# Kernel tuning notes

Hardware: AMD Instinct MI355X
Metric: run time of the kernel (lower is better)

Reference implementation:

```python
import jax, jax.numpy as jnp
import numpy as np

N_NODES = 100000
N_EDGES = 1200000
IN_CH = 64
HID = 64


def sage_conv(x, src, dst, Wl, b, Wr, num_nodes):
    # mean aggregation of source-node features at target nodes (flow=source_to_target)
    msg = x[src]                                      # [E, C] gather
    agg = jax.ops.segment_sum(msg, dst, num_segments=num_nodes)  # [N, C]
    cnt = jax.ops.segment_sum(jnp.ones((src.shape[0],), x.dtype), dst,
                              num_segments=num_nodes)
    mean = agg / jnp.maximum(cnt, 1.0)[:, None]
    # PyG SAGEConv: lin_l(aggregated) + bias + lin_r(root)
    return mean @ Wl + b + x @ Wr


def setup_inputs() -> dict:
    key = jax.random.key(0)
    ks = jax.random.split(key, 10)
    x = jax.random.normal(ks[0], (N_NODES, IN_CH), dtype=jnp.float32)
    edge_index = jax.random.randint(ks[1], (2, N_EDGES), 0, N_NODES, dtype=jnp.int64)
    s1 = 1.0 / np.sqrt(IN_CH)
    s2 = 1.0 / np.sqrt(HID)
    W1l = jax.random.uniform(ks[2], (IN_CH, HID), jnp.float32, -s1, s1)
    b1 = jax.random.uniform(ks[3], (HID,), jnp.float32, -s1, s1)
    W1r = jax.random.uniform(ks[4], (IN_CH, HID), jnp.float32, -s1, s1)
    W2l = jax.random.uniform(ks[5], (HID, HID), jnp.float32, -s2, s2)
    b2 = jax.random.uniform(ks[6], (HID,), jnp.float32, -s2, s2)
    W2r = jax.random.uniform(ks[7], (HID, HID), jnp.float32, -s2, s2)
    Wfc = jax.random.uniform(ks[8], (HID, 1), jnp.float32, -s2, s2)
    bfc = jax.random.uniform(ks[9], (1,), jnp.float32, -s2, s2)
    return {"x": x, "edge_index": edge_index, "W1l": W1l, "b1": b1, "W1r": W1r,
            "W2l": W2l, "b2": b2, "W2r": W2r, "Wfc": Wfc, "bfc": bfc}


def reference(x, edge_index, W1l, b1, W1r, W2l, b2, W2r, Wfc, bfc):
    num_nodes = x.shape[0]
    src, dst = edge_index[0], edge_index[1]
    x = jnp.nan_to_num(x, nan=0.0)
    # layer 1: SAGEConv -> ReLU (dropout is identity in eval)
    h = jax.nn.relu(sage_conv(x, src, dst, W1l, b1, W1r, num_nodes))
    # layer 2
    h = jax.nn.relu(sage_conv(h, src, dst, W2l, b2, W2r, num_nodes))
    pred = (h @ Wfc + bfc)[:, 0]  # (num_nodes,)
    return pred
```

## Files before the change

### kernel.cpp

```cpp
#include <hip/hip_runtime.h>

#define NN_NODES 100000
#define NN_EDGES 1200000
#define CH 64
#define BUCKET_NODES 200
#define NBUCKETS (NN_NODES / BUCKET_NODES)
#define EPB 4096
#define PREP_THREADS 1024
#define XCDS 8
#define PCAP 768
#define BMAX (XCDS * PCAP)

#define PA_BLOCKS ((NN_EDGES + EPB - 1) / EPB)
#define CV_ITEMS (NN_NODES * CH / 4)
#define CV_BLOCKS ((CV_ITEMS + PREP_THREADS - 1) / PREP_THREADS)
#define WP_ITEMS (64 * 128)
#define WP_BLOCKS ((WP_ITEMS + PREP_THREADS - 1) / PREP_THREADS)

typedef __attribute__((ext_vector_type(8))) short bf16x8;
typedef __attribute__((ext_vector_type(4))) float f32x4;

__device__ __forceinline__ float nan0(float v) { return v == v ? v : 0.0f; }

__device__ __forceinline__ unsigned short f2bf(float f) {
    unsigned u = __float_as_uint(f);
    return (unsigned short)((u + 0x7fffu + ((u >> 16) & 1u)) >> 16);
}

__device__ __forceinline__ unsigned xcc_id() {
    unsigned x;
    asm volatile("s_getreg_b32 %0, hwreg(HW_REG_XCC_ID)" : "=s"(x));
    return x & (XCDS - 1);
}

__global__ __launch_bounds__(PREP_THREADS) void prep_kernel(
    const float* __restrict__ x, unsigned short* __restrict__ xb,
    const float* __restrict__ W1l, const float* __restrict__ W1r,
    const float* __restrict__ W2l, const float* __restrict__ W2r,
    unsigned short* __restrict__ Wt1, unsigned short* __restrict__ Wt2,
    const int* __restrict__ src, const int* __restrict__ dst,
    int* __restrict__ bcnt, unsigned int* __restrict__ bbuf)
{
    __shared__ int lhist[NBUCKETS];
    __shared__ int lbase[NBUCKETS];
    int tid = threadIdx.x;
    int bid = blockIdx.x;

    if (bid < PA_BLOCKS) {
        int e0 = bid * EPB;
        unsigned xcc = xcc_id();

        for (int i = tid; i < NBUCKETS; i += PREP_THREADS) lhist[i] = 0;
        __syncthreads();

        int eb = e0 + tid * 4;
        int nv = NN_EDGES - eb;
        if (nv > 4) nv = 4;
        int da[4] = {-1, -1, -1, -1};
        if (nv == 4) {
            int4 dv = *(const int4*)(dst + eb);
            da[0] = dv.x; da[1] = dv.y; da[2] = dv.z; da[3] = dv.w;
        } else {
            for (int r = 0; r < nv; r++) da[r] = dst[eb + r];
        }
        #pragma unroll
        for (int r = 0; r < 4; r++)
            if (da[r] >= 0) atomicAdd(&lhist[da[r] / BUCKET_NODES], 1);
        __syncthreads();

        for (int i = tid; i < NBUCKETS; i += PREP_THREADS) {
            int c = lhist[i];
            lbase[i] = c > 0 ? atomicAdd(&bcnt[i * XCDS + xcc], c) : 0;
            lhist[i] = 0;
        }
        __syncthreads();

        int sa[4] = {0, 0, 0, 0};
        if (nv == 4) {
            int4 sv = *(const int4*)(src + eb);
            sa[0] = sv.x; sa[1] = sv.y; sa[2] = sv.z; sa[3] = sv.w;
        } else {
            for (int r = 0; r < nv; r++) sa[r] = src[eb + r];
        }
        #pragma unroll
        for (int r = 0; r < 4; r++) {
            int d = da[r];
            if (d >= 0) {
                int b = d / BUCKET_NODES;
                int dloc = d - b * BUCKET_NODES;
                int pos = lbase[b] + atomicAdd(&lhist[b], 1);
                if (pos < PCAP)
                    bbuf[((size_t)b * XCDS + xcc) * PCAP + pos] =
                        ((unsigned)dloc << 24) | (unsigned)sa[r];
            }
        }
    } else if (bid < PA_BLOCKS + CV_BLOCKS) {
        int i = (bid - PA_BLOCKS) * PREP_THREADS + tid;
        if (i < CV_ITEMS) {
            float4 v = ((const float4*)x)[i];
            v.x = nan0(v.x); v.y = nan0(v.y); v.z = nan0(v.z); v.w = nan0(v.w);
            ushort4 o;
            o.x = f2bf(v.x); o.y = f2bf(v.y); o.z = f2bf(v.z); o.w = f2bf(v.w);
            ((ushort4*)xb)[i] = o;
        }
    } else {
        int i = (bid - PA_BLOCKS - CV_BLOCKS) * PREP_THREADS + tid;
        if (i < WP_ITEMS) {
            int n = i >> 7;
            int k = i & 127;
            float v1 = (k < 64) ? W1l[k * 64 + n] : W1r[(k - 64) * 64 + n];
            float v2 = (k < 64) ? W2l[k * 64 + n] : W2r[(k - 64) * 64 + n];
            Wt1[i] = f2bf(v1);
            Wt2[i] = f2bf(v2);
        }
    }
}

__global__ __launch_bounds__(256) void passB_kernel(
    const int* __restrict__ bcnt, const unsigned int* __restrict__ bbuf,
    int* __restrict__ col, int* __restrict__ rowptr)
{
    __shared__ int hist[BUCKET_NODES];
    __shared__ int cur[BUCKET_NODES];
    __shared__ int sc[256];
    __shared__ unsigned int stage[BMAX];
    int b = blockIdx.x;
    int t = threadIdx.x;

    for (int i = t; i < BUCKET_NODES; i += 256) hist[i] = 0;

    int part = 0;
    int lim = b * XCDS;
    for (int i = t; i < lim; i += 256) {
        int c = bcnt[i];
        part += c > PCAP ? PCAP : c;
    }
    sc[t] = part;
    __syncthreads();
    #pragma unroll
    for (int off = 128; off > 0; off >>= 1) {
        if (t < off) sc[t] += sc[t + off];
        __syncthreads();
    }
    int base = sc[0];
    __syncthreads();

    int cnt = 0;
    #pragma unroll
    for (int x = 0; x < XCDS; x++) {
        int pc = bcnt[b * XCDS + x];
        if (pc > PCAP) pc = PCAP;
        const unsigned int* seg = bbuf + ((size_t)b * XCDS + x) * PCAP;
        for (int k = t; k < pc; k += 256) {
            unsigned v = seg[k];
            stage[cnt + k] = v;
            atomicAdd(&hist[v >> 24], 1);
        }
        cnt += pc;
    }
    __syncthreads();

    int own = (t < BUCKET_NODES) ? hist[t] : 0;
    sc[t] = own;
    __syncthreads();
    for (int off = 1; off < 256; off <<= 1) {
        int v = (t >= off) ? sc[t - off] : 0;
        __syncthreads();
        sc[t] += v;
        __syncthreads();
    }
    if (t < BUCKET_NODES) {
        int excl = sc[t] - own;
        rowptr[b * BUCKET_NODES + t] = base + excl;
        cur[t] = excl;
    }
    if (b == NBUCKETS - 1 && t == 0) rowptr[NN_NODES] = base + cnt;
    __syncthreads();

    for (int k = t; k < cnt; k += 256) {
        unsigned v = stage[k];
        int dloc = (int)(v >> 24);
        int pos = atomicAdd(&cur[dloc], 1);
        col[base + pos] = (int)(v & 0xFFFFFFu);
    }
}

__global__ __launch_bounds__(256) void gather_kernel(
    const unsigned short* __restrict__ xb,
    const int* __restrict__ rowptr, const int* __restrict__ col,
    unsigned short* __restrict__ mgb, int nNodes)
{
    int w    = threadIdx.x >> 6;
    int lane = threadIdx.x & 63;
    int sub  = lane >> 4;
    int l16  = lane & 15;
    int node = blockIdx.x * 4 + w;
    if (node >= nNodes) return;
    int r0 = rowptr[node], r1 = rowptr[node + 1];
    float a0[4] = {0, 0, 0, 0}, a1[4] = {0, 0, 0, 0};
    int i = r0 + sub;
    for (; i + 4 < r1; i += 8) {
        int s0 = col[i];
        int s1 = col[i + 4];
        uint2 u0 = *(const uint2*)(xb + (size_t)s0 * CH + l16 * 4);
        uint2 u1 = *(const uint2*)(xb + (size_t)s1 * CH + l16 * 4);
        a0[0] += __uint_as_float(u0.x << 16);
        a0[1] += __uint_as_float(u0.x & 0xffff0000u);
        a0[2] += __uint_as_float(u0.y << 16);
        a0[3] += __uint_as_float(u0.y & 0xffff0000u);
        a1[0] += __uint_as_float(u1.x << 16);
        a1[1] += __uint_as_float(u1.x & 0xffff0000u);
        a1[2] += __uint_as_float(u1.y << 16);
        a1[3] += __uint_as_float(u1.y & 0xffff0000u);
    }
    if (i < r1) {
        int s0 = col[i];
        uint2 u0 = *(const uint2*)(xb + (size_t)s0 * CH + l16 * 4);
        a0[0] += __uint_as_float(u0.x << 16);
        a0[1] += __uint_as_float(u0.x & 0xffff0000u);
        a0[2] += __uint_as_float(u0.y << 16);
        a0[3] += __uint_as_float(u0.y & 0xffff0000u);
    }
    #pragma unroll
    for (int j = 0; j < 4; j++) a0[j] += a1[j];
    #pragma unroll
    for (int j = 0; j < 4; j++) {
        a0[j] += __shfl_xor(a0[j], 16, 64);
        a0[j] += __shfl_xor(a0[j], 32, 64);
    }
    if (lane < 16) {
        int deg = r1 - r0;
        float inv = 1.0f / (float)(deg > 0 ? deg : 1);
        ushort4 o;
        o.x = f2bf(a0[0] * inv); o.y = f2bf(a0[1] * inv);
        o.z = f2bf(a0[2] * inv); o.w = f2bf(a0[3] * inv);
        *(ushort4*)(mgb + (size_t)node * CH + l16 * 4) = o;
    }
}

template<int LAYER>
__global__ __launch_bounds__(256) void dense_kernel(
    const unsigned short* __restrict__ rootb,
    const unsigned short* __restrict__ mgb,
    const unsigned short* __restrict__ Wt,
    const float* __restrict__ bias,
    const float* __restrict__ Wfc, const float* __restrict__ bfc,
    unsigned short* __restrict__ hb_out,
    float* __restrict__ out,
    int nNodes)
{
    __shared__ unsigned short sA[64][136];
    __shared__ unsigned short sW[64][136];
    __shared__ unsigned short sO[64][72];

    int tid = threadIdx.x;
    int n_base = blockIdx.x * 64;

    {
        const uint4* g = (const uint4*)Wt;
        for (int i = tid; i < 1024; i += 256) {
            int n = i >> 4;
            int c = i & 15;
            *(uint4*)&sW[n][c * 8] = g[i];
        }
    }
    {
        for (int i = tid; i < 1024; i += 256) {
            int node = i >> 4;
            int c = i & 15;
            int gn = n_base + node;
            if (gn >= nNodes) gn = nNodes - 1;
            const unsigned short* srcp = (c < 8)
                ? (mgb + (size_t)gn * CH + c * 8)
                : (rootb + (size_t)gn * CH + (c - 8) * 8);
            *(uint4*)&sA[node][c * 8] = *(const uint4*)srcp;
        }
    }
    __syncthreads();

    int wave = tid >> 6;
    int lane = tid & 63;
    int quad = lane >> 4;
    int colx = lane & 15;
    int m0 = wave * 16;

    f32x4 acc[4];
    #pragma unroll
    for (int nt = 0; nt < 4; nt++) acc[nt] = (f32x4){0.f, 0.f, 0.f, 0.f};

    #pragma unroll
    for (int ks = 0; ks < 4; ks++) {
        bf16x8 af = *(const bf16x8*)&sA[m0 + colx][ks * 32 + quad * 8];
        #pragma unroll
        for (int nt = 0; nt < 4; nt++) {
            bf16x8 bfr = *(const bf16x8*)&sW[nt * 16 + colx][ks * 32 + quad * 8];
            acc[nt] = __builtin_amdgcn_mfma_f32_16x16x32_bf16(af, bfr, acc[nt], 0, 0, 0);
        }
    }

    float bv[4];
    #pragma unroll
    for (int nt = 0; nt < 4; nt++) bv[nt] = bias[nt * 16 + colx];

    if (LAYER == 1) {
        #pragma unroll
        for (int nt = 0; nt < 4; nt++)
            #pragma unroll
            for (int r = 0; r < 4; r++) {
                float v = acc[nt][r] + bv[nt];
                v = v > 0.f ? v : 0.f;
                sO[m0 + quad * 4 + r][nt * 16 + colx] = f2bf(v);
            }
        __syncthreads();
        for (int i = tid; i < 512; i += 256) {
            int node = i >> 3;
            int c = i & 7;
            int gn = n_base + node;
            if (gn < nNodes)
                *(uint4*)(hb_out + (size_t)gn * CH + c * 8) =
                    *(const uint4*)&sO[node][c * 8];
        }
    } else {
        float wf[4];
        #pragma unroll
        for (int nt = 0; nt < 4; nt++) wf[nt] = Wfc[nt * 16 + colx];
        float bfc0 = bfc[0];
        #pragma unroll
        for (int r = 0; r < 4; r++) {
            float p = 0.f;
            #pragma unroll
            for (int nt = 0; nt < 4; nt++) {
                float v = acc[nt][r] + bv[nt];
                v = v > 0.f ? v : 0.f;
                p += v * wf[nt];
            }
            p += __shfl_xor(p, 1, 64);
            p += __shfl_xor(p, 2, 64);
            p += __shfl_xor(p, 4, 64);
            p += __shfl_xor(p, 8, 64);
            if (colx == 0) {
                int gn = n_base + m0 + quad * 4 + r;
                if (gn < nNodes) out[gn] = p + bfc0;
            }
        }
    }
}

extern "C" void kernel_launch(void* const* d_in, const int* in_sizes, int n_in,
                              void* d_out, int out_size, void* d_ws, size_t ws_size,
                              hipStream_t stream) {
    const float* x    = (const float*)d_in[0];
    const int*   ei   = (const int*)d_in[1];
    const float* W1l  = (const float*)d_in[2];
    const float* b1   = (const float*)d_in[3];
    const float* W1r  = (const float*)d_in[4];
    const float* W2l  = (const float*)d_in[5];
    const float* b2   = (const float*)d_in[6];
    const float* W2r  = (const float*)d_in[7];
    const float* Wfc  = (const float*)d_in[8];
    const float* bfc  = (const float*)d_in[9];
    float* out = (float*)d_out;

    const int N = NN_NODES;
    const int E = NN_EDGES;
    const int* src = ei;
    const int* dst = ei + E;

    char* ws = (char*)d_ws;
    unsigned short* xb  = (unsigned short*)ws;  ws += (size_t)N * CH * sizeof(unsigned short);
    unsigned short* h1b = (unsigned short*)ws;  ws += (size_t)N * CH * sizeof(unsigned short);
    unsigned short* mgb = (unsigned short*)ws;  ws += (size_t)N * CH * sizeof(unsigned short);
    unsigned short* Wt1 = (unsigned short*)ws;  ws += 64 * 128 * sizeof(unsigned short);
    unsigned short* Wt2 = (unsigned short*)ws;  ws += 64 * 128 * sizeof(unsigned short);
    int* bcnt   = (int*)ws;                     ws += (size_t)NBUCKETS * XCDS * sizeof(int);
    int* rowptr = (int*)ws;                     ws += (size_t)(N + 1) * sizeof(int);
    int* col    = (int*)ws;                     ws += (size_t)E * sizeof(int);
    unsigned int* bbuf = (unsigned int*)mgb;

    hipMemsetAsync(bcnt, 0, (size_t)NBUCKETS * XCDS * sizeof(int), stream);

    prep_kernel<<<PA_BLOCKS + CV_BLOCKS + WP_BLOCKS, PREP_THREADS, 0, stream>>>(
        x, xb, W1l, W1r, W2l, W2r, Wt1, Wt2, src, dst, bcnt, bbuf);
    passB_kernel<<<NBUCKETS, 256, 0, stream>>>(bcnt, bbuf, col, rowptr);

    int gblocks = (N + 3) / 4;
    int dblocks = (N + 63) / 64;

    gather_kernel<<<gblocks, 256, 0, stream>>>(xb, rowptr, col, mgb, N);
    dense_kernel<1><<<dblocks, 256, 0, stream>>>(
        xb, mgb, Wt1, b1, nullptr, nullptr, h1b, nullptr, N);
    gather_kernel<<<gblocks, 256, 0, stream>>>(h1b, rowptr, col, mgb, N);
    dense_kernel<2><<<dblocks, 256, 0, stream>>>(
        h1b, mgb, Wt2, b2, Wfc, bfc, nullptr, out, N);
}
```

Baseline: 214.5 us.

## Fuse neighbor mean-gather with dense SAGE layer into one kernel per layer

Merges the gather kernel and the MFMA dense kernel for each layer into a single kernel. Each block handles 16 nodes, gathers their neighbour means straight into shared memory, and then runs the 128x64 matmul with one wave per 16-column output tile. This removes the intermediate mgb buffer write and read and two kernel launches. In exchange, every block reloads the full 16 KB weight tile for only 16 nodes, and layer 2 now reduces through shared-memory atomics.

```diff
diff --git a/kernel.cpp b/kernel.cpp
--- a/kernel.cpp
+++ b/kernel.cpp
@@ -16,6 +16,9 @@
 #define CV_BLOCKS ((CV_ITEMS + PREP_THREADS - 1) / PREP_THREADS)
 #define WP_ITEMS (64 * 128)
 #define WP_BLOCKS ((WP_ITEMS + PREP_THREADS - 1) / PREP_THREADS)
+
+#define FUSED_NODES 16
+#define FUSED_BLOCKS (NN_NODES / FUSED_NODES)
 
 typedef __attribute__((ext_vector_type(8))) short bf16x8;
 typedef __attribute__((ext_vector_type(4))) float f32x4;
@@ -185,76 +188,23 @@
     }
 }
 
-__global__ __launch_bounds__(256) void gather_kernel(
-    const unsigned short* __restrict__ xb,
+template<int LAYER>
+__global__ __launch_bounds__(256) void fused_kernel(
+    const unsigned short* __restrict__ feat,
     const int* __restrict__ rowptr, const int* __restrict__ col,
-    unsigned short* __restrict__ mgb, int nNodes)
-{
-    int w    = threadIdx.x >> 6;
-    int lane = threadIdx.x & 63;
-    int sub  = lane >> 4;
-    int l16  = lane & 15;
-    int node = blockIdx.x * 4 + w;
-    if (node >= nNodes) return;
-    int r0 = rowptr[node], r1 = rowptr[node + 1];
-    float a0[4] = {0, 0, 0, 0}, a1[4] = {0, 0, 0, 0};
-    int i = r0 + sub;
-    for (; i + 4 < r1; i += 8) {
-        int s0 = col[i];
-        int s1 = col[i + 4];
-        uint2 u0 = *(const uint2*)(xb + (size_t)s0 * CH + l16 * 4);
-        uint2 u1 = *(const uint2*)(xb + (size_t)s1 * CH + l16 * 4);
-        a0[0] += __uint_as_float(u0.x << 16);
-        a0[1] += __uint_as_float(u0.x & 0xffff0000u);
-        a0[2] += __uint_as_float(u0.y << 16);
-        a0[3] += __uint_as_float(u0.y & 0xffff0000u);
-        a1[0] += __uint_as_float(u1.x << 16);
-        a1[1] += __uint_as_float(u1.x & 0xffff0000u);
-        a1[2] += __uint_as_float(u1.y << 16);
-        a1[3] += __uint_as_float(u1.y & 0xffff0000u);
-    }
-    if (i < r1) {
-        int s0 = col[i];
-        uint2 u0 = *(const uint2*)(xb + (size_t)s0 * CH + l16 * 4);
-        a0[0] += __uint_as_float(u0.x << 16);
-        a0[1] += __uint_as_float(u0.x & 0xffff0000u);
-        a0[2] += __uint_as_float(u0.y << 16);
-        a0[3] += __uint_as_float(u0.y & 0xffff0000u);
-    }
-    #pragma unroll
-    for (int j = 0; j < 4; j++) a0[j] += a1[j];
-    #pragma unroll
-    for (int j = 0; j < 4; j++) {
-        a0[j] += __shfl_xor(a0[j], 16, 64);
-        a0[j] += __shfl_xor(a0[j], 32, 64);
-    }
-    if (lane < 16) {
-        int deg = r1 - r0;
-        float inv = 1.0f / (float)(deg > 0 ? deg : 1);
-        ushort4 o;
-        o.x = f2bf(a0[0] * inv); o.y = f2bf(a0[1] * inv);
-        o.z = f2bf(a0[2] * inv); o.w = f2bf(a0[3] * inv);
-        *(ushort4*)(mgb + (size_t)node * CH + l16 * 4) = o;
-    }
-}
-
-template<int LAYER>
-__global__ __launch_bounds__(256) void dense_kernel(
-    const unsigned short* __restrict__ rootb,
-    const unsigned short* __restrict__ mgb,
     const unsigned short* __restrict__ Wt,
     const float* __restrict__ bias,
     const float* __restrict__ Wfc, const float* __restrict__ bfc,
     unsigned short* __restrict__ hb_out,
-    float* __restrict__ out,
-    int nNodes)
+    float* __restrict__ out)
 {
-    __shared__ unsigned short sA[64][136];
+    __shared__ unsigned short sA[FUSED_NODES][136];
     __shared__ unsigned short sW[64][136];
-    __shared__ unsigned short sO[64][72];
+    __shared__ unsigned short sO[FUSED_NODES][72];
+    __shared__ float psum[FUSED_NODES];
 
     int tid = threadIdx.x;
-    int n_base = blockIdx.x * 64;
+    int n_base = blockIdx.x * FUSED_NODES;
 
     {
         const uint4* g = (const uint4*)Wt;
@@ -264,85 +214,114 @@
             *(uint4*)&sW[n][c * 8] = g[i];
         }
     }
-    {
-        for (int i = tid; i < 1024; i += 256) {
-            int node = i >> 4;
-            int c = i & 15;
-            int gn = n_base + node;
-            if (gn >= nNodes) gn = nNodes - 1;
-            const unsigned short* srcp = (c < 8)
-                ? (mgb + (size_t)gn * CH + c * 8)
-                : (rootb + (size_t)gn * CH + (c - 8) * 8);
-            *(uint4*)&sA[node][c * 8] = *(const uint4*)srcp;
-        }
-    }
-    __syncthreads();
-
-    int wave = tid >> 6;
+    for (int i = tid; i < FUSED_NODES * 8; i += 256) {
+        int node = i >> 3;
+        int c = i & 7;
+        *(uint4*)&sA[node][64 + c * 8] =
+            *(const uint4*)(feat + (size_t)(n_base + node) * CH + c * 8);
+    }
+    if (LAYER == 2 && tid < FUSED_NODES) psum[tid] = 0.f;
+
+    int w    = tid >> 6;
     int lane = tid & 63;
+    int sub  = lane >> 4;
+    int l16  = lane & 15;
+
+    int r0a[4], r1a[4];
+    #pragma unroll
+    for (int j = 0; j < 4; j++) {
+        int node = n_base + w * 4 + j;
+        r0a[j] = rowptr[node];
+        r1a[j] = rowptr[node + 1];
+    }
+
+    #pragma unroll
+    for (int j = 0; j < 4; j++) {
+        int nl = w * 4 + j;
+        int r0 = r0a[j], r1 = r1a[j];
+        float a0[4] = {0, 0, 0, 0}, a1[4] = {0, 0, 0, 0};
+        int i = r0 + sub;
+        for (; i + 4 < r1; i += 8) {
+            int s0 = col[i];
+            int s1 = col[i + 4];
+            uint2 u0 = *(const uint2*)(feat + (size_t)s0 * CH + l16 * 4);
+            uint2 u1 = *(const uint2*)(feat + (size_t)s1 * CH + l16 * 4);
+            a0[0] += __uint_as_float(u0.x << 16);
+            a0[1] += __uint_as_float(u0.x & 0xffff0000u);
+            a0[2] += __uint_as_float(u0.y << 16);
+            a0[3] += __uint_as_float(u0.y & 0xffff0000u);
+            a1[0] += __uint_as_float(u1.x << 16);
+            a1[1] += __uint_as_float(u1.x & 0xffff0000u);
+            a1[2] += __uint_as_float(u1.y << 16);
+            a1[3] += __uint_as_float(u1.y & 0xffff0000u);
+        }
+        if (i < r1) {
+            int s0 = col[i];
+            uint2 u0 = *(const uint2*)(feat + (size_t)s0 * CH + l16 * 4);
+            a0[0] += __uint_as_float(u0.x << 16);
+            a0[1] += __uint_as_float(u0.x & 0xffff0000u);
+            a0[2] += __uint_as_float(u0.y << 16);
+            a0[3] += __uint_as_float(u0.y & 0xffff0000u);
+        }
+        #pragma unroll
+        for (int q = 0; q < 4; q++) a0[q] += a1[q];
+        #pragma unroll
+        for (int q = 0; q < 4; q++) {
+            a0[q] += __shfl_xor(a0[q], 16, 64);
+            a0[q] += __shfl_xor(a0[q], 32, 64);
+        }
+        if (lane < 16) {
+            int deg = r1 - r0;
+            float inv = 1.0f / (float)(deg > 0 ? deg : 1);
+            ushort4 o;
+            o.x = f2bf(a0[0] * inv); o.y = f2bf(a0[1] * inv);
+            o.z = f2bf(a0[2] * inv); o.w = f2bf(a0[3] * inv);
+            *(ushort4*)&sA[nl][l16 * 4] = o;
+        }
+    }
+    __syncthreads();
+
     int quad = lane >> 4;
     int colx = lane & 15;
-    int m0 = wave * 16;
-
-    f32x4 acc[4];
-    #pragma unroll
-    for (int nt = 0; nt < 4; nt++) acc[nt] = (f32x4){0.f, 0.f, 0.f, 0.f};
-
+
+    f32x4 acc = (f32x4){0.f, 0.f, 0.f, 0.f};
     #pragma unroll
     for (int ks = 0; ks < 4; ks++) {
-        bf16x8 af = *(const bf16x8*)&sA[m0 + colx][ks * 32 + quad * 8];
-        #pragma unroll
-        for (int nt = 0; nt < 4; nt++) {
-            bf16x8 bfr = *(const bf16x8*)&sW[nt * 16 + colx][ks * 32 + quad * 8];
-            acc[nt] = __builtin_amdgcn_mfma_f32_16x16x32_bf16(af, bfr, acc[nt], 0, 0, 0);
-        }
-    }
-
-    float bv[4];
-    #pragma unroll
-    for (int nt = 0; nt < 4; nt++) bv[nt] = bias[nt * 16 + colx];
+        bf16x8 af  = *(const bf16x8*)&sA[colx][ks * 32 + quad * 8];
+        bf16x8 bfr = *(const bf16x8*)&sW[w * 16 + colx][ks * 32 + quad * 8];
+        acc = __builtin_amdgcn_mfma_f32_16x16x32_bf16(af, bfr, acc, 0, 0, 0);
+    }
+    float bv = bias[w * 16 + colx];
 
     if (LAYER == 1) {
         #pragma unroll
-        for (int nt = 0; nt < 4; nt++)
-            #pragma unroll
-            for (int r = 0; r < 4; r++) {
-                float v = acc[nt][r] + bv[nt];
-                v = v > 0.f ? v : 0.f;
-                sO[m0 + quad * 4 + r][nt * 16 + colx] = f2bf(v);
-            }
-        __syncthreads();
-        for (int i = tid; i < 512; i += 256) {
+        for (int r = 0; r < 4; r++) {
+            float v = acc[r] + bv;
+            v = v > 0.f ? v : 0.f;
+            sO[quad * 4 + r][w * 16 + colx] = f2bf(v);
+        }
+        __syncthreads();
+        for (int i = tid; i < FUSED_NODES * 8; i += 256) {
             int node = i >> 3;
             int c = i & 7;
-            int gn = n_base + node;
-            if (gn < nNodes)
-                *(uint4*)(hb_out + (size_t)gn * CH + c * 8) =
-                    *(const uint4*)&sO[node][c * 8];
+            *(uint4*)(hb_out + (size_t)(n_base + node) * CH + c * 8) =
+                *(const uint4*)&sO[node][c * 8];
         }
     } else {
-        float wf[4];
-        #pragma unroll
-        for (int nt = 0; nt < 4; nt++) wf[nt] = Wfc[nt * 16 + colx];
-        float bfc0 = bfc[0];
+        float wf = Wfc[w * 16 + colx];
         #pragma unroll
         for (int r = 0; r < 4; r++) {
-            float p = 0.f;
-            #pragma unroll
-            for (int nt = 0; nt < 4; nt++) {
-                float v = acc[nt][r] + bv[nt];
-                v = v > 0.f ? v : 0.f;
-                p += v * wf[nt];
-            }
+            float v = acc[r] + bv;
+            v = v > 0.f ? v : 0.f;
+            float p = v * wf;
             p += __shfl_xor(p, 1, 64);
             p += __shfl_xor(p, 2, 64);
             p += __shfl_xor(p, 4, 64);
             p += __shfl_xor(p, 8, 64);
-            if (colx == 0) {
-                int gn = n_base + m0 + quad * 4 + r;
-                if (gn < nNodes) out[gn] = p + bfc0;
-            }
-        }
+            if (colx == 0) atomicAdd(&psum[quad * 4 + r], p);
+        }
+        __syncthreads();
+        if (tid < FUSED_NODES) out[n_base + tid] = psum[tid] + bfc[0];
     }
 }
 
@@ -369,13 +348,12 @@
     char* ws = (char*)d_ws;
     unsigned short* xb  = (unsigned short*)ws;  ws += (size_t)N * CH * sizeof(unsigned short);
     unsigned short* h1b = (unsigned short*)ws;  ws += (size_t)N * CH * sizeof(unsigned short);
-    unsigned short* mgb = (unsigned short*)ws;  ws += (size_t)N * CH * sizeof(unsigned short);
     unsigned short* Wt1 = (unsigned short*)ws;  ws += 64 * 128 * sizeof(unsigned short);
     unsigned short* Wt2 = (unsigned short*)ws;  ws += 64 * 128 * sizeof(unsigned short);
     int* bcnt   = (int*)ws;                     ws += (size_t)NBUCKETS * XCDS * sizeof(int);
     int* rowptr = (int*)ws;                     ws += (size_t)(N + 1) * sizeof(int);
     int* col    = (int*)ws;                     ws += (size_t)E * sizeof(int);
-    unsigned int* bbuf = (unsigned int*)mgb;
+    unsigned int* bbuf = (unsigned int*)ws;     ws += (size_t)NBUCKETS * XCDS * PCAP * sizeof(unsigned int);
 
     hipMemsetAsync(bcnt, 0, (size_t)NBUCKETS * XCDS * sizeof(int), stream);
 
@@ -383,13 +361,8 @@
         x, xb, W1l, W1r, W2l, W2r, Wt1, Wt2, src, dst, bcnt, bbuf);
     passB_kernel<<<NBUCKETS, 256, 0, stream>>>(bcnt, bbuf, col, rowptr);
 
-    int gblocks = (N + 3) / 4;
-    int dblocks = (N + 63) / 64;
-
-    gather_kernel<<<gblocks, 256, 0, stream>>>(xb, rowptr, col, mgb, N);
-    dense_kernel<1><<<dblocks, 256, 0, stream>>>(
-        xb, mgb, Wt1, b1, nullptr, nullptr, h1b, nullptr, N);
-    gather_kernel<<<gblocks, 256, 0, stream>>>(h1b, rowptr, col, mgb, N);
-    dense_kernel<2><<<dblocks, 256, 0, stream>>>(
-        h1b, mgb, Wt2, b2, Wfc, bfc, nullptr, out, N);
-}
+    fused_kernel<1><<<FUSED_BLOCKS, 256, 0, stream>>>(
+        xb, rowptr, col, Wt1, b1, nullptr, nullptr, h1b, nullptr);
+    fused_kernel<2><<<FUSED_BLOCKS, 256, 0, stream>>>(
+        h1b, rowptr, col, Wt2, b2, Wfc, bfc, nullptr, out);
+}
```

Result: no change. 213.1 us (-0.6%).
